# Kernel optimization log

Measured on AMD Instinct MI355X. Metric: run time of the kernel, lower is better.

Reference implementation:

```python
import jax, jax.numpy as jnp
import numpy as np

N_USERS = 200_000
N_ITEMS = 100_000
N_NODES = N_USERS + N_ITEMS
EMB = 100          # emb_size; transForm1 in_features=200 == 2*EMB
NNZ = 1_000_000    # raw user-item interactions
BATCH = 16_384
N_LAYERS = 4


def _build_norm_adj(rng):
    """Replicates get_norm_adj_mat: symmetric bipartite adjacency + self-loops,
    D^-0.5 A D^-0.5 normalization. Returns COO (row, col, vals)."""
    uid = rng.integers(0, N_USERS, NNZ).astype(np.int64)
    iid = rng.integers(0, N_ITEMS, NNZ).astype(np.int64) + N_USERS
    # dok_matrix dict-update dedupes repeated (u,i) pairs
    pair_key = uid * N_NODES + iid
    _, keep = np.unique(pair_key, return_index=True)
    uid, iid = uid[keep], iid[keep]
    loops = np.arange(N_NODES, dtype=np.int64)
    row = np.concatenate([uid, iid, loops])
    col = np.concatenate([iid, uid, loops])
    deg = np.bincount(row, minlength=N_NODES).astype(np.float32)  # (A>0) row sums
    dinv = deg ** -0.5
    vals = dinv[row] * dinv[col]
    return row.astype(np.int32), col.astype(np.int32), vals.astype(np.float32)


def setup_inputs() -> dict:
    key = jax.random.key(0)
    ks = jax.random.split(key, 16)
    rng = np.random.default_rng(0)
    adj_row, adj_col, adj_vals = _build_norm_adj(rng)

    def lin(k, fan_in, fan_out):
        # torch Linear default init: U(-1/sqrt(fan_in), 1/sqrt(fan_in))
        bound = 1.0 / np.sqrt(fan_in)
        kw, kb = jax.random.split(k)
        W = jax.random.uniform(kw, (fan_in, fan_out), jnp.float32, -bound, bound)
        b = jax.random.uniform(kb, (fan_out,), jnp.float32, -bound, bound)
        return W, b

    W1, b1 = lin(ks[0], 200, 128)
    W4, b4 = lin(ks[1], 128, 64)
    W2, b2 = lin(ks[2], 64, 32)
    W3, b3 = lin(ks[3], 32, 1)

    return {
        "userIdx": jax.random.randint(ks[4], (BATCH,), 0, N_USERS, jnp.int32),
        "itemIdx": jax.random.randint(ks[5], (BATCH,), 0, N_ITEMS, jnp.int32),
        "adj_row": jnp.asarray(adj_row),
        "adj_col": jnp.asarray(adj_col),
        "adj_vals": jnp.asarray(adj_vals),
        "user_emb": jax.random.normal(ks[6], (N_USERS, EMB), jnp.float32),
        "item_emb": jax.random.normal(ks[7], (N_ITEMS, EMB), jnp.float32),
        "W1": W1, "b1": b1, "W4": W4, "b4": b4,
        "W2": W2, "b2": b2, "W3": W3, "b3": b3,
        "u_bias": jax.random.normal(ks[8], (N_USERS, 1), jnp.float32),
        "i_bias": jax.random.normal(ks[9], (N_USERS + N_ITEMS, 1), jnp.float32),
    }


def reference(userIdx, itemIdx, adj_row, adj_col, adj_vals,
              user_emb, item_emb, W1, b1, W4, b4, W2, b2, W3, b3,
              u_bias, i_bias):
    item_nodes = itemIdx + N_USERS
    # LightGCN propagation: 4 sparse SpMM layers, mean over {0..4} embeddings
    emb = jnp.concatenate([user_emb, item_emb], axis=0)   # [N_NODES, EMB]
    acc = emb
    x = emb
    for _ in range(N_LAYERS):
        x = jax.ops.segment_sum(adj_vals[:, None] * x[adj_col], adj_row,
                                num_segments=N_NODES)
        acc = acc + x
    final = acc / float(N_LAYERS + 1)

    u = final[userIdx]          # [B, EMB]
    i = final[item_nodes]       # [B, EMB]
    h = jnp.concatenate([u, i], axis=1)          # [B, 200]
    h = jax.nn.relu(h @ W1 + b1)                 # transForm1 + ReLU
    h = h @ W4 + b4                              # transForm4
    h = h @ W2 + b2                              # transForm2
    h = h @ W3 + b3                              # transForm3 -> [B, 1]
    bias = u_bias[userIdx, 0] + i_bias[item_nodes, 0]
    return h.ravel() + bias
```

## Files before the change

### kernel.cpp

```cpp
#include <hip/hip_runtime.h>
#include <hip/hip_bf16.h>

#define N_USERS 200000
#define N_ITEMS 100000
#define N_NODES 300000
#define EMB 100
#define XSTRIDE 64
#define BATCH 16384
#define UNR 8
#define NROWBLK (N_NODES / 4)
#define NRIDER (BATCH / 4)

#define SCAN_BLK 1024
#define NBLK ((N_NODES + SCAN_BLK - 1) / SCAN_BLK)

__device__ __forceinline__ unsigned int f2bf(float f) {
    unsigned int x = __float_as_uint(f);
    return (x + 0x7fffu + ((x >> 16) & 1u)) >> 16;
}
__device__ __forceinline__ float bf_lo(unsigned int u) { return __uint_as_float(u << 16); }
__device__ __forceinline__ float bf_hi(unsigned int u) { return __uint_as_float(u & 0xffff0000u); }


__global__ void hist_copy_kernel(const int* __restrict__ row, const int* __restrict__ col,
                                 const float* __restrict__ val, int* __restrict__ cnt,
                                 int2* __restrict__ cedge, int Eu) {
    for (int i = blockIdx.x * blockDim.x + threadIdx.x; i < 2 * Eu;
         i += gridDim.x * blockDim.x) {
        atomicAdd(&cnt[row[i]], 1);
        if (i < Eu) cedge[i] = make_int2(col[i], __float_as_int(val[i]));
    }
}

__global__ __launch_bounds__(SCAN_BLK) void block_reduce_kernel(const int* __restrict__ cnt,
                                                                int* __restrict__ bsum, int n) {
    __shared__ int sm[SCAN_BLK];
    int i = blockIdx.x * SCAN_BLK + threadIdx.x;
    sm[threadIdx.x] = (i < n) ? cnt[i] : 0;
    __syncthreads();
    for (int off = SCAN_BLK / 2; off > 0; off >>= 1) {
        if (threadIdx.x < off) sm[threadIdx.x] += sm[threadIdx.x + off];
        __syncthreads();
    }
    if (threadIdx.x == 0) bsum[blockIdx.x] = sm[0];
}

__global__ __launch_bounds__(512) void scan_bsum_kernel(int* __restrict__ bsum,
                                                        int* __restrict__ rp_total) {
    __shared__ int sm[512];
    int v = (threadIdx.x < NBLK) ? bsum[threadIdx.x] : 0;
    sm[threadIdx.x] = v;
    __syncthreads();
    for (int off = 1; off < 512; off <<= 1) {
        int t = (threadIdx.x >= off) ? sm[threadIdx.x - off] : 0;
        __syncthreads();
        sm[threadIdx.x] += t;
        __syncthreads();
    }
    if (threadIdx.x < NBLK) bsum[threadIdx.x] = sm[threadIdx.x] - v;
    if (threadIdx.x == 511) rp_total[0] = sm[511];
}

__global__ __launch_bounds__(SCAN_BLK) void block_scan_kernel(const int* __restrict__ cnt,
                                                              const int* __restrict__ bsum,
                                                              int* __restrict__ rp,
                                                              int* __restrict__ cur, int n) {
    __shared__ int sm[SCAN_BLK];
    int i = blockIdx.x * SCAN_BLK + threadIdx.x;
    int v = (i < n) ? cnt[i] : 0;
    sm[threadIdx.x] = v;
    __syncthreads();
    for (int off = 1; off < SCAN_BLK; off <<= 1) {
        int t = (threadIdx.x >= off) ? sm[threadIdx.x - off] : 0;
        __syncthreads();
        sm[threadIdx.x] += t;
        __syncthreads();
    }
    if (i < n) {
        int x = bsum[blockIdx.x] + sm[threadIdx.x] - v;
        rp[i] = x;
        if (i >= N_USERS) cur[i] = x;
    }
}

__global__ void scatter_item_kernel(const int* __restrict__ row, const int* __restrict__ col,
                                    const float* __restrict__ val, int* __restrict__ cur,
                                    int2* __restrict__ cedge, int Eu) {
    for (int i = blockIdx.x * blockDim.x + threadIdx.x; i < Eu; i += gridDim.x * blockDim.x) {
        int ii = Eu + i;
        int r = row[ii];
        int p = atomicAdd(&cur[r], 1);
        cedge[p] = make_int2(col[ii], __float_as_int(val[ii]));
    }
}


__global__ __launch_bounds__(256) void conv_kernel(const float* __restrict__ user_emb,
                                                   const float* __restrict__ item_emb,
                                                   unsigned int* __restrict__ x,
                                                   const int* __restrict__ uidx,
                                                   const int* __restrict__ iidx,
                                                   float* __restrict__ acc) {
    int bid = blockIdx.x;
    int wv = threadIdx.x >> 6, lane = threadIdx.x & 63;
    if (bid >= NROWBLK) {
        int b = (bid - NROWBLK) * 4 + wv;
        if (lane >= 50) return;
        const float2* ur = (const float2*)(user_emb + (unsigned)uidx[b] * EMB);
        const float2* ir = (const float2*)(item_emb + (unsigned)iidx[b] * EMB);
        float2* a2 = (float2*)(acc + (unsigned)b * 200);
        a2[lane] = ur[lane];
        a2[50 + lane] = ir[lane];
        return;
    }
    int node = bid * 4 + wv;
    unsigned int u = 0;
    if (lane < 50) {
        const float* src = (node < N_USERS) ? (user_emb + (unsigned)node * EMB)
                                            : (item_emb + (unsigned)(node - N_USERS) * EMB);
        float2 v = ((const float2*)src)[lane];
        u = f2bf(v.x) | (f2bf(v.y) << 16);
    }
    x[((unsigned)node << 6) + lane] = u;
}


__global__ __launch_bounds__(256) void spmm_kernel(const int* __restrict__ rp,
                                                   const int2* __restrict__ cedge,
                                                   const float* __restrict__ vloop,
                                                   const unsigned int* __restrict__ xin,
                                                   unsigned int* __restrict__ xout,
                                                   const int* __restrict__ uidx,
                                                   const int* __restrict__ iidx,
                                                   float* __restrict__ acc) {
    int bid = blockIdx.x;
    int wv = threadIdx.x >> 6, lane = threadIdx.x & 63;
    if (bid >= NROWBLK) {
        int b = (bid - NROWBLK) * 4 + wv;
        if (lane >= 50) return;
        unsigned int uu = xin[((unsigned)uidx[b] << 6) + lane];
        unsigned int iu = xin[(((unsigned)iidx[b] + N_USERS) << 6) + lane];
        float2* a2 = (float2*)(acc + (unsigned)b * 200);
        float2 o0 = a2[lane], o1 = a2[50 + lane];
        a2[lane] = make_float2(o0.x + bf_lo(uu), o0.y + bf_hi(uu));
        a2[50 + lane] = make_float2(o1.x + bf_lo(iu), o1.y + bf_hi(iu));
        return;
    }
    int row = __builtin_amdgcn_readfirstlane(bid * 4 + wv);
    int s = rp[row], e = rp[row + 1];
    float vl = vloop[row];
    unsigned int urow = xin[((unsigned)row << 6) + lane];
    float ax = vl * bf_lo(urow), ay = vl * bf_hi(urow);
    for (int j0 = s; j0 < e; j0 += UNR) {
        int n = e - j0;
        int2 ed[UNR];
        #pragma unroll
        for (int k = 0; k < UNR; ++k)
            ed[k] = cedge[j0 + ((k < n) ? k : 0)];
        unsigned int u[UNR];
        #pragma unroll
        for (int k = 0; k < UNR; ++k)
            u[k] = xin[((unsigned)ed[k].x << 6) + lane];
        #pragma unroll
        for (int k = 0; k < UNR; ++k) {
            float v = (k < n) ? __int_as_float(ed[k].y) : 0.f;
            ax += v * bf_lo(u[k]);
            ay += v * bf_hi(u[k]);
        }
    }
    xout[((unsigned)row << 6) + lane] = f2bf(ax) | (f2bf(ay) << 16);
}


__global__ __launch_bounds__(256) void batch_spmm_kernel(const int* __restrict__ rp,
        const int2* __restrict__ cedge, const float* __restrict__ vloop,
        const unsigned int* __restrict__ xin,
        const int* __restrict__ uidx, const int* __restrict__ iidx,
        float* __restrict__ acc) {
    int t = blockIdx.x * 4 + (threadIdx.x >> 6);
    int lane = threadIdx.x & 63;
    int b = t >> 1, half = t & 1;
    int row = __builtin_amdgcn_readfirstlane(half ? (iidx[b] + N_USERS) : uidx[b]);
    int s = rp[row], e = rp[row + 1];
    float vl = vloop[row] + 1.0f;
    unsigned int urow = xin[((unsigned)row << 6) + lane];
    float ax = vl * bf_lo(urow), ay = vl * bf_hi(urow);
    for (int j0 = s; j0 < e; j0 += UNR) {
        int n = e - j0;
        int2 ed[UNR];
        #pragma unroll
        for (int k = 0; k < UNR; ++k)
            ed[k] = cedge[j0 + ((k < n) ? k : 0)];
        unsigned int u[UNR];
        #pragma unroll
        for (int k = 0; k < UNR; ++k)
            u[k] = xin[((unsigned)ed[k].x << 6) + lane];
        #pragma unroll
        for (int k = 0; k < UNR; ++k) {
            float v = (k < n) ? __int_as_float(ed[k].y) : 0.f;
            ax += v * bf_lo(u[k]);
            ay += v * bf_hi(u[k]);
        }
    }
    if (lane < 50) {
        float2* arow = (float2*)(acc + (unsigned)b * 200 + half * 100);
        float2 old = arow[lane];
        arow[lane] = make_float2(old.x + ax, old.y + ay);
    }
}


__global__ __launch_bounds__(512) void mlp_kernel(const float* __restrict__ acc,
        const float* __restrict__ W1, const float* __restrict__ b1,
        const float* __restrict__ W4, const float* __restrict__ b4,
        const float* __restrict__ W2, const float* __restrict__ b2,
        const float* __restrict__ W3, const float* __restrict__ b3,
        const int* __restrict__ uidx, const int* __restrict__ iidx,
        const float* __restrict__ u_bias, const float* __restrict__ i_bias,
        float* __restrict__ out) {
    __shared__ float W1s[200 * 128];
    __shared__ float in_s[8][2][200];
    __shared__ float h1_s[8][2][128];
    __shared__ float h2_s[8][2][64];
    int tid = threadIdx.x;
    for (int i = tid; i < 200 * 128 / 4; i += 512)
        ((float4*)W1s)[i] = ((const float4*)W1)[i];
    __syncthreads();

    int w = tid >> 6, lane = tid & 63;
    int row0 = blockIdx.x * 64 + w * 8;
    for (int pr = 0; pr < 4; ++pr) {
        int ba = row0 + pr * 2, bb = ba + 1;
        for (int t = lane; t < 200; t += 64) {
            in_s[w][0][t] = acc[(unsigned)ba * 200 + t] * 0.2f;
            in_s[w][1][t] = acc[(unsigned)bb * 200 + t] * 0.2f;
        }
        {
            float s0a = b1[lane], s1a = b1[64 + lane];
            float s0b = s0a, s1b = s1a;
            for (int k = 0; k < 200; ++k) {
                float wa = W1s[k * 128 + lane], wb = W1s[k * 128 + 64 + lane];
                float ia = in_s[w][0][k], ib = in_s[w][1][k];
                s0a += ia * wa; s1a += ia * wb;
                s0b += ib * wa; s1b += ib * wb;
            }
            h1_s[w][0][lane] = fmaxf(s0a, 0.f);
            h1_s[w][0][64 + lane] = fmaxf(s1a, 0.f);
            h1_s[w][1][lane] = fmaxf(s0b, 0.f);
            h1_s[w][1][64 + lane] = fmaxf(s1b, 0.f);
        }
        {
            float sa = b4[lane], sb = sa;
            for (int k = 0; k < 128; ++k) {
                float wv = W4[k * 64 + lane];
                sa += h1_s[w][0][k] * wv;
                sb += h1_s[w][1][k] * wv;
            }
            h2_s[w][0][lane] = sa;
            h2_s[w][1][lane] = sb;
        }
        float pa = 0.f, pb = 0.f;
        if (lane < 32) {
            float sa = b2[lane], sb = sa;
            for (int k = 0; k < 64; ++k) {
                float wv = W2[k * 32 + lane];
                sa += h2_s[w][0][k] * wv;
                sb += h2_s[w][1][k] * wv;
            }
            float w3 = W3[lane];
            pa = sa * w3;
            pb = sb * w3;
        }
        #pragma unroll
        for (int off = 16; off >= 1; off >>= 1) {
            pa += __shfl_xor(pa, off);
            pb += __shfl_xor(pb, off);
        }
        if (lane == 0) {
            out[ba] = pa + b3[0] + u_bias[uidx[ba]] + i_bias[iidx[ba] + N_USERS];
            out[bb] = pb + b3[0] + u_bias[uidx[bb]] + i_bias[iidx[bb] + N_USERS];
        }
    }
}


extern "C" void kernel_launch(void* const* d_in, const int* in_sizes, int n_in,
                              void* d_out, int out_size, void* d_ws, size_t ws_size,
                              hipStream_t stream) {
    const int*   userIdx  = (const int*)d_in[0];
    const int*   itemIdx  = (const int*)d_in[1];
    const int*   adj_row  = (const int*)d_in[2];
    const int*   adj_col  = (const int*)d_in[3];
    const float* adj_vals = (const float*)d_in[4];
    const float* user_emb = (const float*)d_in[5];
    const float* item_emb = (const float*)d_in[6];
    const float* W1 = (const float*)d_in[7],  *b1 = (const float*)d_in[8];
    const float* W4 = (const float*)d_in[9],  *b4 = (const float*)d_in[10];
    const float* W2 = (const float*)d_in[11], *b2 = (const float*)d_in[12];
    const float* W3 = (const float*)d_in[13], *b3 = (const float*)d_in[14];
    const float* u_bias = (const float*)d_in[15];
    const float* i_bias = (const float*)d_in[16];
    const int E = in_sizes[2];
    const int Eu = (E - N_NODES) / 2;
    const float* vloop = adj_vals + (size_t)2 * Eu;

    char* ws = (char*)d_ws;
    size_t off = 0;
    auto carve = [&](size_t bytes) -> char* {
        char* p = ws + off;
        off += (bytes + 255) & ~(size_t)255;
        return p;
    };
    int*   rp    = (int*)  carve((size_t)(N_NODES + 1) * sizeof(int));
    int*   cur   = (int*)  carve((size_t)N_NODES * sizeof(int));
    int*   bsum  = (int*)  carve((size_t)NBLK * sizeof(int));
    int2*  cedge = (int2*) carve((size_t)2 * Eu * sizeof(int2));
    unsigned int* x0 = (unsigned int*)carve((size_t)N_NODES * XSTRIDE * 4);
    unsigned int* x1 = (unsigned int*)carve((size_t)N_NODES * XSTRIDE * 4);
    float* accb  = (float*)carve((size_t)BATCH * 2 * EMB * sizeof(float));
    (void)ws_size; (void)n_in; (void)out_size;

    hipMemsetAsync(cur, 0, (size_t)N_NODES * sizeof(int), stream);
    hist_copy_kernel<<<2048, 256, 0, stream>>>(adj_row, adj_col, adj_vals, cur, cedge, Eu);
    block_reduce_kernel<<<NBLK, SCAN_BLK, 0, stream>>>(cur, bsum, N_NODES);
    scan_bsum_kernel<<<1, 512, 0, stream>>>(bsum, rp + N_NODES);
    block_scan_kernel<<<NBLK, SCAN_BLK, 0, stream>>>(cur, bsum, rp, cur, N_NODES);
    scatter_item_kernel<<<2048, 256, 0, stream>>>(adj_row, adj_col, adj_vals, cur, cedge, Eu);

    conv_kernel<<<NROWBLK + NRIDER, 256, 0, stream>>>(user_emb, item_emb, x0,
                                                      userIdx, itemIdx, accb);

    spmm_kernel<<<NROWBLK, 256, 0, stream>>>(rp, cedge, vloop, x0, x1,
                                             userIdx, itemIdx, accb);
    spmm_kernel<<<NROWBLK + NRIDER, 256, 0, stream>>>(rp, cedge, vloop, x1, x0,
                                                      userIdx, itemIdx, accb);
    spmm_kernel<<<NROWBLK + NRIDER, 256, 0, stream>>>(rp, cedge, vloop, x0, x1,
                                                      userIdx, itemIdx, accb);

    batch_spmm_kernel<<<2 * BATCH / 4, 256, 0, stream>>>(rp, cedge, vloop, x1,
                                                         userIdx, itemIdx, accb);

    mlp_kernel<<<BATCH / 64, 512, 0, stream>>>(accb, W1, b1, W4, b4, W2, b2, W3, b3,
                                               userIdx, itemIdx, u_bias, i_bias,
                                               (float*)d_out);
}
```

Measured before the change: 737.4 us.

## Fuse CSR build with embedding conversion; derive user row pointers from sorted rows

The user half of the edge list is sorted by row, so the user row pointers are now computed directly from row boundaries instead of by histogram and scan. The histogram and scan now cover only item rows. The histogram, user-rowptr fill, bf16 conversion and batch gather are merged into one launch to cut launch count and let the phases overlap. Nontemporal stores are added for the bf16 embedding writes. This relies on the user-side edges being sorted by row (true for the np.unique construction), which is an assumption about the input layout.

```diff
diff --git a/kernel.cpp b/kernel.cpp
--- a/kernel.cpp
+++ b/kernel.cpp
@@ -10,9 +10,11 @@
 #define UNR 8
 #define NROWBLK (N_NODES / 4)
 #define NRIDER (BATCH / 4)
+#define HBLK 2048
+#define UBBLK 2048
 
 #define SCAN_BLK 1024
-#define NBLK ((N_NODES + SCAN_BLK - 1) / SCAN_BLK)
+#define NBLK_I ((N_ITEMS + SCAN_BLK - 1) / SCAN_BLK)
 
 __device__ __forceinline__ unsigned int f2bf(float f) {
     unsigned int x = __float_as_uint(f);
@@ -21,22 +23,67 @@
 __device__ __forceinline__ float bf_lo(unsigned int u) { return __uint_as_float(u << 16); }
 __device__ __forceinline__ float bf_hi(unsigned int u) { return __uint_as_float(u & 0xffff0000u); }
 
-
-__global__ void hist_copy_kernel(const int* __restrict__ row, const int* __restrict__ col,
-                                 const float* __restrict__ val, int* __restrict__ cnt,
-                                 int2* __restrict__ cedge, int Eu) {
-    for (int i = blockIdx.x * blockDim.x + threadIdx.x; i < 2 * Eu;
-         i += gridDim.x * blockDim.x) {
-        atomicAdd(&cnt[row[i]], 1);
-        if (i < Eu) cedge[i] = make_int2(col[i], __float_as_int(val[i]));
-    }
-}
+__global__ __launch_bounds__(256) void phase1_kernel(
+        const int* __restrict__ row, const int* __restrict__ col,
+        const float* __restrict__ val, int* __restrict__ cnt,
+        int2* __restrict__ cedge, int* __restrict__ rp,
+        const float* __restrict__ user_emb, const float* __restrict__ item_emb,
+        unsigned int* __restrict__ x,
+        const int* __restrict__ uidx, const int* __restrict__ iidx,
+        float* __restrict__ acc, int Eu) {
+    int bid = blockIdx.x;
+    if (bid < HBLK) {
+        for (int i = bid * 256 + threadIdx.x; i < Eu; i += HBLK * 256) {
+            atomicAdd(&cnt[row[Eu + i] - N_USERS], 1);
+            cedge[i] = make_int2(col[i], __float_as_int(val[i]));
+        }
+        return;
+    }
+    bid -= HBLK;
+    if (bid < UBBLK) {
+        for (int i = bid * 256 + threadIdx.x; i < Eu; i += UBBLK * 256) {
+            int r = row[i];
+            if (i == 0) {
+                for (int q = 0; q <= r; ++q) rp[q] = 0;
+            } else {
+                int pr = row[i - 1];
+                for (int q = pr + 1; q <= r; ++q) rp[q] = i;
+            }
+            if (i == Eu - 1)
+                for (int q = r + 1; q <= N_USERS; ++q) rp[q] = Eu;
+        }
+        return;
+    }
+    bid -= UBBLK;
+    int wv = threadIdx.x >> 6, lane = threadIdx.x & 63;
+    if (bid < NROWBLK) {
+        int node = bid * 4 + wv;
+        unsigned int u = 0;
+        if (lane < 50) {
+            const float* src = (node < N_USERS) ? (user_emb + (unsigned)node * EMB)
+                                                : (item_emb + (unsigned)(node - N_USERS) * EMB);
+            float2 v = ((const float2*)src)[lane];
+            u = f2bf(v.x) | (f2bf(v.y) << 16);
+        }
+        __builtin_nontemporal_store(u, &x[((unsigned)node << 6) + lane]);
+        return;
+    }
+    bid -= NROWBLK;
+    int b = bid * 4 + wv;
+    if (lane >= 50) return;
+    const float2* ur = (const float2*)(user_emb + (unsigned)uidx[b] * EMB);
+    const float2* ir = (const float2*)(item_emb + (unsigned)iidx[b] * EMB);
+    float2* a2 = (float2*)(acc + (unsigned)b * 200);
+    a2[lane] = ur[lane];
+    a2[50 + lane] = ir[lane];
+}
+
 
 __global__ __launch_bounds__(SCAN_BLK) void block_reduce_kernel(const int* __restrict__ cnt,
-                                                                int* __restrict__ bsum, int n) {
+                                                                int* __restrict__ bsum) {
     __shared__ int sm[SCAN_BLK];
     int i = blockIdx.x * SCAN_BLK + threadIdx.x;
-    sm[threadIdx.x] = (i < n) ? cnt[i] : 0;
+    sm[threadIdx.x] = (i < N_ITEMS) ? cnt[i] : 0;
     __syncthreads();
     for (int off = SCAN_BLK / 2; off > 0; off >>= 1) {
         if (threadIdx.x < off) sm[threadIdx.x] += sm[threadIdx.x + off];
@@ -45,29 +92,29 @@
     if (threadIdx.x == 0) bsum[blockIdx.x] = sm[0];
 }
 
-__global__ __launch_bounds__(512) void scan_bsum_kernel(int* __restrict__ bsum,
-                                                        int* __restrict__ rp_total) {
-    __shared__ int sm[512];
-    int v = (threadIdx.x < NBLK) ? bsum[threadIdx.x] : 0;
+__global__ __launch_bounds__(128) void scan_bsum_kernel(int* __restrict__ bsum,
+                                                        int* __restrict__ rp_last, int Eu) {
+    __shared__ int sm[128];
+    int v = (threadIdx.x < NBLK_I) ? bsum[threadIdx.x] : 0;
     sm[threadIdx.x] = v;
     __syncthreads();
-    for (int off = 1; off < 512; off <<= 1) {
+    for (int off = 1; off < 128; off <<= 1) {
         int t = (threadIdx.x >= off) ? sm[threadIdx.x - off] : 0;
         __syncthreads();
         sm[threadIdx.x] += t;
         __syncthreads();
     }
-    if (threadIdx.x < NBLK) bsum[threadIdx.x] = sm[threadIdx.x] - v;
-    if (threadIdx.x == 511) rp_total[0] = sm[511];
+    if (threadIdx.x < NBLK_I) bsum[threadIdx.x] = sm[threadIdx.x] - v;
+    if (threadIdx.x == 127) rp_last[0] = Eu + sm[127];
 }
 
 __global__ __launch_bounds__(SCAN_BLK) void block_scan_kernel(const int* __restrict__ cnt,
                                                               const int* __restrict__ bsum,
                                                               int* __restrict__ rp,
-                                                              int* __restrict__ cur, int n) {
+                                                              int* __restrict__ cur, int Eu) {
     __shared__ int sm[SCAN_BLK];
     int i = blockIdx.x * SCAN_BLK + threadIdx.x;
-    int v = (i < n) ? cnt[i] : 0;
+    int v = (i < N_ITEMS) ? cnt[i] : 0;
     sm[threadIdx.x] = v;
     __syncthreads();
     for (int off = 1; off < SCAN_BLK; off <<= 1) {
@@ -76,10 +123,10 @@
         sm[threadIdx.x] += t;
         __syncthreads();
     }
-    if (i < n) {
-        int x = bsum[blockIdx.x] + sm[threadIdx.x] - v;
-        rp[i] = x;
-        if (i >= N_USERS) cur[i] = x;
+    if (i < N_ITEMS) {
+        int x = Eu + bsum[blockIdx.x] + sm[threadIdx.x] - v;
+        rp[N_USERS + i] = x;
+        cur[i] = x;
     }
 }
 
@@ -88,40 +135,9 @@
                                     int2* __restrict__ cedge, int Eu) {
     for (int i = blockIdx.x * blockDim.x + threadIdx.x; i < Eu; i += gridDim.x * blockDim.x) {
         int ii = Eu + i;
-        int r = row[ii];
-        int p = atomicAdd(&cur[r], 1);
+        int p = atomicAdd(&cur[row[ii] - N_USERS], 1);
         cedge[p] = make_int2(col[ii], __float_as_int(val[ii]));
     }
-}
-
-
-__global__ __launch_bounds__(256) void conv_kernel(const float* __restrict__ user_emb,
-                                                   const float* __restrict__ item_emb,
-                                                   unsigned int* __restrict__ x,
-                                                   const int* __restrict__ uidx,
-                                                   const int* __restrict__ iidx,
-                                                   float* __restrict__ acc) {
-    int bid = blockIdx.x;
-    int wv = threadIdx.x >> 6, lane = threadIdx.x & 63;
-    if (bid >= NROWBLK) {
-        int b = (bid - NROWBLK) * 4 + wv;
-        if (lane >= 50) return;
-        const float2* ur = (const float2*)(user_emb + (unsigned)uidx[b] * EMB);
-        const float2* ir = (const float2*)(item_emb + (unsigned)iidx[b] * EMB);
-        float2* a2 = (float2*)(acc + (unsigned)b * 200);
-        a2[lane] = ur[lane];
-        a2[50 + lane] = ir[lane];
-        return;
-    }
-    int node = bid * 4 + wv;
-    unsigned int u = 0;
-    if (lane < 50) {
-        const float* src = (node < N_USERS) ? (user_emb + (unsigned)node * EMB)
-                                            : (item_emb + (unsigned)(node - N_USERS) * EMB);
-        float2 v = ((const float2*)src)[lane];
-        u = f2bf(v.x) | (f2bf(v.y) << 16);
-    }
-    x[((unsigned)node << 6) + lane] = u;
 }
 
 
@@ -168,7 +184,8 @@
             ay += v * bf_hi(u[k]);
         }
     }
-    xout[((unsigned)row << 6) + lane] = f2bf(ax) | (f2bf(ay) << 16);
+    unsigned int o = f2bf(ax) | (f2bf(ay) << 16);
+    __builtin_nontemporal_store(o, &xout[((unsigned)row << 6) + lane]);
 }
 
 
@@ -312,23 +329,23 @@
         return p;
     };
     int*   rp    = (int*)  carve((size_t)(N_NODES + 1) * sizeof(int));
-    int*   cur   = (int*)  carve((size_t)N_NODES * sizeof(int));
-    int*   bsum  = (int*)  carve((size_t)NBLK * sizeof(int));
+    int*   cnt   = (int*)  carve((size_t)N_ITEMS * sizeof(int));
+    int*   bsum  = (int*)  carve((size_t)NBLK_I * sizeof(int));
     int2*  cedge = (int2*) carve((size_t)2 * Eu * sizeof(int2));
     unsigned int* x0 = (unsigned int*)carve((size_t)N_NODES * XSTRIDE * 4);
     unsigned int* x1 = (unsigned int*)carve((size_t)N_NODES * XSTRIDE * 4);
     float* accb  = (float*)carve((size_t)BATCH * 2 * EMB * sizeof(float));
     (void)ws_size; (void)n_in; (void)out_size;
 
-    hipMemsetAsync(cur, 0, (size_t)N_NODES * sizeof(int), stream);
-    hist_copy_kernel<<<2048, 256, 0, stream>>>(adj_row, adj_col, adj_vals, cur, cedge, Eu);
-    block_reduce_kernel<<<NBLK, SCAN_BLK, 0, stream>>>(cur, bsum, N_NODES);
-    scan_bsum_kernel<<<1, 512, 0, stream>>>(bsum, rp + N_NODES);
-    block_scan_kernel<<<NBLK, SCAN_BLK, 0, stream>>>(cur, bsum, rp, cur, N_NODES);
-    scatter_item_kernel<<<2048, 256, 0, stream>>>(adj_row, adj_col, adj_vals, cur, cedge, Eu);
-
-    conv_kernel<<<NROWBLK + NRIDER, 256, 0, stream>>>(user_emb, item_emb, x0,
-                                                      userIdx, itemIdx, accb);
+    hipMemsetAsync(cnt, 0, (size_t)N_ITEMS * sizeof(int), stream);
+    phase1_kernel<<<HBLK + UBBLK + NROWBLK + NRIDER, 256, 0, stream>>>(
+        adj_row, adj_col, adj_vals, cnt, cedge, rp,
+        user_emb, item_emb, x0, userIdx, itemIdx, accb, Eu);
+
+    block_reduce_kernel<<<NBLK_I, SCAN_BLK, 0, stream>>>(cnt, bsum);
+    scan_bsum_kernel<<<1, 128, 0, stream>>>(bsum, rp + N_NODES, Eu);
+    block_scan_kernel<<<NBLK_I, SCAN_BLK, 0, stream>>>(cnt, bsum, rp, cnt, Eu);
+    scatter_item_kernel<<<2048, 256, 0, stream>>>(adj_row, adj_col, adj_vals, cnt, cedge, Eu);
 
     spmm_kernel<<<NROWBLK, 256, 0, stream>>>(rp, cedge, vloop, x0, x1,
                                              userIdx, itemIdx, accb);
```

After: 738.9 us. Within noise of the previous version (+0.2%).
